# Kernel tuning notes

Hardware: AMD Instinct MI355X
Metric: run time of the kernel (lower is better)

## Reference

```python
import jax, jax.numpy as jnp
import numpy as np
import math

NUM_HEADS = 16
SEGMENT_SIZE = 256
DILATION_RATE = 2


def _hilbert_curve(n):
    if n == 1:
        return [(0, 0)]
    m = n // 2
    sub = _hilbert_curve(m)
    pts = [(y, x) for (x, y) in sub]
    pts += [(x, y + m) for (x, y) in sub]
    pts += [(x + m, y + m) for (x, y) in sub]
    pts += [(m - 1 - y + m, m - 1 - x) for (x, y) in sub]
    return pts


def generate_hilbert_curve_mapping(seq_len):
    grid = 2 ** int(math.ceil(math.log2(math.sqrt(seq_len))))
    pts = _hilbert_curve(grid)
    lin2hil = np.zeros(seq_len, dtype=np.int32)
    for h_idx, (x, y) in enumerate(pts[:seq_len]):
        lin = y * grid + x
        if lin < seq_len:
            lin2hil[lin] = h_idx
    return lin2hil


def setup_inputs() -> dict:
    key = jax.random.key(0)
    k1, k2, k3 = jax.random.split(key, 3)
    B, S, H = 1, 4096, 2048
    scale = H ** -0.5
    x = jax.random.normal(k1, (B, S, H), dtype=jnp.float32)
    w_qkv = jax.random.normal(k2, (3 * H, H), dtype=jnp.float32) * scale
    w_out = jax.random.normal(k3, (H, H), dtype=jnp.float32) * scale
    hilbert_map = jnp.asarray(generate_hilbert_curve_mapping(S))
    return {"x": x, "w_qkv": w_qkv, "w_out": w_out, "hilbert_map": hilbert_map}


def _kv_positions(S, seg, dil):
    # Union of per-segment dilated positions: seg_start + j*dil (< segment end).
    seg_starts = np.arange(0, S, seg)
    within = np.arange(0, seg, dil)
    return jnp.asarray((seg_starts[:, None] + within[None, :]).reshape(-1))


def reference(x, w_qkv, w_out, hilbert_map):
    B, S, H = x.shape
    nh = NUM_HEADS
    hd = H // nh
    qkv = x @ w_qkv.T                              # [B,S,3H]
    qkv = qkv.reshape(B, S, 3, nh, hd).transpose(2, 0, 3, 1, 4)  # [3,B,nh,S,hd]
    q, k, v = qkv[0], qkv[1], qkv[2]

    kv_pos = _kv_positions(S, SEGMENT_SIZE, DILATION_RATE)  # [Nk]
    gathered = hilbert_map[kv_pos]                 # Hilbert-mapped KV indices
    kg = k[:, :, gathered, :]                      # [B,nh,Nk,hd]
    vg = v[:, :, gathered, :]

    scale = 1.0 / jnp.sqrt(jnp.float32(hd))
    scores = jnp.einsum("bhmd,bhnd->bhmn", q, kg) * scale
    p = jax.nn.softmax(scores, axis=-1)
    acc = jnp.einsum("bhmn,bhnd->bhmd", p, vg)     # [B,nh,S,hd]

    # Scatter: out[:, :, hilbert_map[m], :] = acc[:, :, m, :]
    out = jnp.zeros_like(acc).at[:, :, hilbert_map, :].set(acc)
    out = out.transpose(0, 2, 1, 3).reshape(B, S, H)
    return out @ w_out.T
```

## Files before the change

kernel.cpp:

```cpp
#include <hip/hip_runtime.h>
#include <math.h>

#define S_LEN 4096
#define HID   2048
#define NH    16
#define HD    128
#define NKV   2048
#define KT    64
#define QBLK  256
#define NT    (NKV / KT)
#define QSCALE 0.12754103668587426f

typedef __attribute__((ext_vector_type(8))) _Float16 half8;
typedef __attribute__((ext_vector_type(4))) _Float16 half4;
typedef __attribute__((ext_vector_type(2))) __fp16 fp16x2;
typedef __attribute__((ext_vector_type(4))) float f32x4;
typedef __attribute__((ext_vector_type(16))) float f32x16;

#define GLB_AS __attribute__((address_space(1)))
#define LDS_AS __attribute__((address_space(3)))

#if __has_builtin(__builtin_amdgcn_exp2f)
#define EXP2(x) __builtin_amdgcn_exp2f(x)
#else
#define EXP2(x) exp2f(x)
#endif

__device__ __forceinline__ void gload16(const void* g, void* l) {
  __builtin_amdgcn_global_load_lds((GLB_AS const void*)g, (LDS_AS void*)l, 16, 0, 0);
}

__device__ __forceinline__ unsigned pkrtz(float a, float b) {
  union { fp16x2 h; unsigned u; } cv;
  cv.h = __builtin_amdgcn_cvt_pkrtz(a, b);
  return cv.u;
}

__global__ void k_build_idx(const int* __restrict__ hmap, int* __restrict__ gidx) {
  int i = blockIdx.x * 256 + threadIdx.x;
  if (i < NKV) gidx[i] = hmap[2 * i];
}

#define NX8  (S_LEN * HID / 8)
#define NW8  (3 * HID * HID / 8)
#define NO8  (HID * HID / 8)
__global__ void k_cvt_all(const float* __restrict__ x, const float* __restrict__ wq,
                          const float* __restrict__ wo, _Float16* __restrict__ x16,
                          _Float16* __restrict__ wq16, _Float16* __restrict__ wo16) {
  int i = blockIdx.x * 256 + threadIdx.x;
  const float* src; _Float16* dst; int j;
  if (i < NX8)            { src = x;  dst = x16;  j = i; }
  else if (i < NX8 + NW8) { src = wq; dst = wq16; j = i - NX8; }
  else                    { src = wo; dst = wo16; j = i - NX8 - NW8; }
  float4 a = ((const float4*)src)[2 * j];
  float4 b = ((const float4*)src)[2 * j + 1];
  half8 h;
  h[0] = (_Float16)a.x; h[1] = (_Float16)a.y; h[2] = (_Float16)a.z; h[3] = (_Float16)a.w;
  h[4] = (_Float16)b.x; h[5] = (_Float16)b.y; h[6] = (_Float16)b.z; h[7] = (_Float16)b.w;
  ((half8*)dst)[j] = h;
}

__global__ __launch_bounds__(512, 2)
void k_gemm_qkv8(const _Float16* __restrict__ A, const _Float16* __restrict__ wqkv,
                 _Float16* __restrict__ q16, const int* __restrict__ gidx,
                 char* __restrict__ kimg, char* __restrict__ vtimg)
{
  extern __shared__ __align__(16) char lds[];
  const int tid = threadIdx.x;
  const int w = tid >> 6, lane = tid & 63;
  const int l15 = lane & 15, l4 = lane >> 4;
  const int wr = w >> 2, wc = w & 3;
  const int K = HID;

  const int bid = (blockIdx.x & 7) * 32 + (blockIdx.x >> 3);
  const bool qpart = bid < 128;
  int m0, n0;
  const _Float16* B;
  if (qpart) { int b = bid;       m0 = (b >> 3) * 256; n0 = (b & 7) * 256;  B = wqkv; }
  else       { int b = bid - 128; m0 = (b >> 4) * 256; n0 = (b & 15) * 256; B = wqkv + (size_t)HID * HID; }

  const int r8 = lane >> 3;
  const int sl = (lane & 7) ^ r8;
  const _Float16* ApA[2][2];
  const _Float16* BpB[2][2];
#pragma unroll
  for (int mh = 0; mh < 2; ++mh)
#pragma unroll
    for (int L = 0; L < 2; ++L) {
      int rel = L * 128 + mh * 64 + w * 8 + r8;
      int grow = qpart ? (m0 + rel) : gidx[m0 + rel];
      ApA[mh][L] = A + (size_t)grow * K + sl * 8;
    }
#pragma unroll
  for (int nh = 0; nh < 2; ++nh)
#pragma unroll
    for (int L = 0; L < 2; ++L) {
      int row = n0 + (L * 2 + (w >> 2)) * 64 + nh * 32 + (w & 3) * 8 + r8;
      BpB[nh][L] = B + (size_t)row * K + sl * 8;
    }

  const int sw0 = (l4 ^ (l15 & 7)) * 16;
  const int sw1 = ((4 + l4) ^ (l15 & 7)) * 16;
  const int rofs = l15 * 128;

  f32x4 acc[8][4];
#pragma unroll
  for (int i = 0; i < 8; ++i)
#pragma unroll
    for (int j = 0; j < 4; ++j) acc[i][j] = (f32x4){0.f, 0.f, 0.f, 0.f};
  half8 af[4][2], bf[2][2];

#define STG_A(MH, BUF, T)                                                       \
  do {                                                                          \
    gload16(ApA[MH][0] + (T) * 64, lds + (BUF)*65536 + (MH)*16384 + w * 1024);  \
    gload16(ApA[MH][1] + (T) * 64, lds + (BUF)*65536 + (MH)*16384 + 8192 + w * 1024); \
  } while (0)
#define STG_B(NH, BUF, T)                                                       \
  do {                                                                          \
    gload16(BpB[NH][0] + (T) * 64, lds + (BUF)*65536 + 32768 + (NH)*16384 + w * 1024); \
    gload16(BpB[NH][1] + (T) * 64, lds + (BUF)*65536 + 32768 + (NH)*16384 + 8192 + w * 1024); \
  } while (0)

#define PH(BUF, MH, NH, LA, LB, STG, WAITS)                                     \
  do {                                                                          \
    if (LA) {                                                                   \
      _Pragma("unroll")                                                         \
      for (int j = 0; j < 4; ++j) {                                             \
        af[j][0] = *(const half8*)(lds + (BUF)*65536 + (MH)*16384 + wr * 8192 + j * 2048 + rofs + sw0); \
        af[j][1] = *(const half8*)(lds + (BUF)*65536 + (MH)*16384 + wr * 8192 + j * 2048 + rofs + sw1); \
      }                                                                         \
    }                                                                           \
    if (LB) {                                                                   \
      _Pragma("unroll")                                                         \
      for (int jn = 0; jn < 2; ++jn) {                                          \
        bf[jn][0] = *(const half8*)(lds + (BUF)*65536 + 32768 + (NH)*16384 + wc * 4096 + jn * 2048 + rofs + sw0); \
        bf[jn][1] = *(const half8*)(lds + (BUF)*65536 + 32768 + (NH)*16384 + wc * 4096 + jn * 2048 + rofs + sw1); \
      }                                                                         \
    }                                                                           \
    STG;                                                                        \
    __builtin_amdgcn_s_barrier();                                               \
    __builtin_amdgcn_s_setprio(1);                                              \
    _Pragma("unroll")                                                           \
    for (int j = 0; j < 4; ++j)                                                 \
      _Pragma("unroll")                                                         \
      for (int jn = 0; jn < 2; ++jn)                                            \
        _Pragma("unroll")                                                       \
        for (int ks = 0; ks < 2; ++ks)                                          \
          acc[(MH)*4 + j][(NH)*2 + jn] = __builtin_amdgcn_mfma_f32_16x16x32_f16( \
              af[j][ks], bf[jn][ks], acc[(MH)*4 + j][(NH)*2 + jn], 0, 0, 0);    \
    __builtin_amdgcn_s_setprio(0);                                              \
    WAITS;                                                                      \
    __builtin_amdgcn_s_barrier();                                               \
  } while (0)

  STG_A(0, 0, 0); STG_B(1, 0, 0); STG_A(1, 0, 0); STG_B(0, 0, 0);
  STG_A(0, 1, 1); STG_B(1, 1, 1);
  asm volatile("s_waitcnt vmcnt(4)");
  __builtin_amdgcn_s_barrier();

  for (int i = 0; i < 15; ++i) {
    const int T1 = 2 * i + 1, T2 = 2 * i + 2, T3 = 2 * i + 3;
    PH(0, 0, 0, 1, 1, STG_A(1, 1, T1), (void)0);
    PH(0, 0, 1, 0, 1, STG_B(0, 1, T1), (void)0);
    PH(0, 1, 1, 1, 0, STG_A(0, 0, T2), (void)0);
    PH(0, 1, 0, 0, 1, STG_B(1, 0, T2), asm volatile("s_waitcnt vmcnt(4)"));
    PH(1, 0, 0, 1, 1, STG_A(1, 0, T2), (void)0);
    PH(1, 0, 1, 0, 1, STG_B(0, 0, T2), (void)0);
    PH(1, 1, 1, 1, 0, STG_A(0, 1, T3), (void)0);
    PH(1, 1, 0, 0, 1, STG_B(1, 1, T3), asm volatile("s_waitcnt vmcnt(4)"));
  }
  PH(0, 0, 0, 1, 1, STG_A(1, 1, 31), (void)0);
  PH(0, 0, 1, 0, 1, STG_B(0, 1, 31), (void)0);
  PH(0, 1, 1, 1, 0, (void)0, (void)0);
  PH(0, 1, 0, 0, 1, (void)0, asm volatile("s_waitcnt vmcnt(0)"));
  PH(1, 0, 0, 1, 1, (void)0, (void)0);
  PH(1, 0, 1, 0, 1, (void)0, (void)0);
  PH(1, 1, 1, 1, 0, (void)0, (void)0);
  PH(1, 1, 0, 0, 1, (void)0, (void)0);
#undef PH
#undef STG_A
#undef STG_B

#pragma unroll
  for (int mf = 0; mf < 8; ++mf)
#pragma unroll
    for (int nf = 0; nf < 4; ++nf)
#pragma unroll
      for (int e = 0; e < 4; ++e) {
        int row = m0 + wr * 128 + mf * 16 + l4 * 4 + e;
        int col = n0 + wc * 64 + nf * 16 + l15;
        _Float16 val = (_Float16)acc[mf][nf][e];
        if (qpart) {
          q16[(size_t)row * HID + col] = val;
        } else {
          int r = row - m0 + m0;
          int t = r >> 6, j = r & 63;
          if (col < HID) {
            int h = col >> 7, d = col & 127;
            int off = (h * 32 + t) * 16384 + ((j * 256 + 2 * d) ^ ((j & 7) << 4));
            *(_Float16*)(kimg + off) = val;
          } else {
            int nn = col - HID;
            int h = nn >> 7, d = nn & 127;
            int off = (h * 32 + t) * 16384 + ((d * 128 + 2 * j) ^ ((d & 7) << 4));
            *(_Float16*)(vtimg + off) = val;
          }
        }
      }
}

__global__ __launch_bounds__(256)
void k_gemm_out(const _Float16* __restrict__ A, const _Float16* __restrict__ B,
                float* __restrict__ C, int M, int N, int K)
{
  __shared__ __align__(16) char Asl[16384];
  __shared__ __align__(16) char Bsl[16384];
  const int tid = threadIdx.x;
  const int w = tid >> 6, lane = tid & 63;
  const int l15 = lane & 15, l4 = lane >> 4;
  const int m0 = blockIdx.y * 128, n0 = blockIdx.x * 128;
  const int wr = w >> 1, wc = w & 1;

  const int srow  = lane >> 3;
  const int kso   = ((lane & 7) ^ srow) * 8;
  const _Float16* Ap[4];
  const _Float16* Bp[4];
#pragma unroll
  for (int q = 0; q < 4; ++q) {
    int row = m0 + 32 * w + 8 * q + srow;
    Ap[q] = A + (size_t)row * K + kso;
    Bp[q] = B + (size_t)(n0 + 32 * w + 8 * q + srow) * K + kso;
  }

  f32x4 acc[4][4];
#pragma unroll
  for (int i = 0; i < 4; ++i)
#pragma unroll
    for (int j = 0; j < 4; ++j) acc[i][j] = (f32x4){0.f, 0.f, 0.f, 0.f};

#define STAGE_T(k0)                                                  \
  do {                                                               \
    _Pragma("unroll")                                                \
    for (int q = 0; q < 4; ++q) {                                    \
      gload16(Ap[q] + (k0), Asl + (4 * w + q) * 1024 + lane * 16);   \
      gload16(Bp[q] + (k0), Bsl + (4 * w + q) * 1024 + lane * 16);   \
    }                                                                \
  } while (0)

  STAGE_T(0);
  __syncthreads();

  const int nt = K >> 6;
  for (int t = 0; t < nt; ++t) {
    half8 af[4][2], bf[4][2];
#pragma unroll
    for (int mi = 0; mi < 4; ++mi) {
      int row = wr * 64 + mi * 16 + l15;
#pragma unroll
      for (int ks = 0; ks < 2; ++ks)
        af[mi][ks] = *(const half8*)(Asl + row * 128 + (((ks * 4 + l4) ^ (row & 7)) * 16));
    }
#pragma unroll
    for (int ni = 0; ni < 4; ++ni) {
      int row = wc * 64 + ni * 16 + l15;
#pragma unroll
      for (int ks = 0; ks < 2; ++ks)
        bf[ni][ks] = *(const half8*)(Bsl + row * 128 + (((ks * 4 + l4) ^ (row & 7)) * 16));
    }
    __syncthreads();
    if (t + 1 < nt) STAGE_T((t + 1) * 64);
    __builtin_amdgcn_s_setprio(1);
#pragma unroll
    for (int mi = 0; mi < 4; ++mi)
#pragma unroll
      for (int ni = 0; ni < 4; ++ni)
#pragma unroll
        for (int ks = 0; ks < 2; ++ks)
          acc[mi][ni] = __builtin_amdgcn_mfma_f32_16x16x32_f16(af[mi][ks], bf[ni][ks], acc[mi][ni], 0, 0, 0);
    __builtin_amdgcn_s_setprio(0);
    __syncthreads();
  }
#undef STAGE_T

  const int rbase = m0 + wr * 64 + l4 * 4;
  const int cbase = n0 + wc * 64 + l15;
#pragma unroll
  for (int mi = 0; mi < 4; ++mi)
#pragma unroll
    for (int ni = 0; ni < 4; ++ni)
#pragma unroll
      for (int e = 0; e < 4; ++e)
        C[(size_t)(rbase + mi * 16 + e) * N + cbase + ni * 16] = acc[mi][ni][e];
}

__global__ __launch_bounds__(512, 2)
void k_attn9(const _Float16* __restrict__ qmat, const char* __restrict__ kimg,
             const char* __restrict__ vtimg, const int* __restrict__ hmap,
             _Float16* __restrict__ att)
{
  extern __shared__ __align__(16) char lds[];
  const int tid = threadIdx.x;
  const int w = tid >> 6, lane = tid & 63;
  const int l31 = lane & 31;
  const bool hi = (lane >> 5) != 0;
  const int hib = hi ? 1 : 0;
  const int work = (blockIdx.x & 7) * 32 + (blockIdx.x >> 3);
  const int h  = work >> 4;
  const int q0 = (work & 15) * QBLK;

  half8 qf[8];
  {
    const int qrow = q0 + w * 32 + l31;
    const _Float16* qb = qmat + (size_t)qrow * HID + h * HD + hib * 8;
    const _Float16 qs = (_Float16)QSCALE;
#pragma unroll
    for (int dk = 0; dk < 8; ++dk) {
      half8 v = *(const half8*)(qb + 16 * dk);
#pragma unroll
      for (int q = 0; q < 8; ++q) v[q] *= qs;
      qf[dk] = v;
    }
  }

  const int swz = (l31 & 7) << 4;
  int koff[4], voff[4];
#pragma unroll
  for (int i = 0; i < 4; ++i) {
    koff[i] = l31 * 256 + ((i * 32 + hib * 16) ^ swz);
    voff[i] = 16384 + l31 * 128 + ((i * 32 + hib * 16) ^ swz);
  }

  const char* kbase = kimg  + (size_t)h * NT * 16384;
  const char* vbase = vtimg + (size_t)h * NT * 16384;

  f32x16 acc[4];
#pragma unroll
  for (int dt = 0; dt < 4; ++dt)
#pragma unroll
    for (int r = 0; r < 16; ++r) acc[dt][r] = 0.f;
  float lsum = 0.f;

#define STAGE(buf, t)                                                          \
  do {                                                                         \
    const char* ks_ = kbase + (size_t)(t) * 16384;                             \
    const char* vs_ = vbase + (size_t)(t) * 16384;                             \
    char* d_ = lds + (buf) * 32768;                                            \
    gload16(ks_ + w * 1024 + lane * 16,          d_ + w * 1024);               \
    gload16(ks_ + (8 + w) * 1024 + lane * 16,    d_ + (8 + w) * 1024);         \
    gload16(vs_ + w * 1024 + lane * 16,          d_ + 16384 + w * 1024);       \
    gload16(vs_ + (8 + w) * 1024 + lane * 16,    d_ + 16384 + (8 + w) * 1024); \
  } while (0)

#define SM_HALF(S, PPK)                                                        \
  do {                                                                         \
    float p_[16];                                                              \
    _Pragma("unroll")                                                          \
    for (int r = 0; r < 16; ++r) { p_[r] = EXP2((S)[r]); lsum += p_[r]; }      \
    _Pragma("unroll")                                                          \
    for (int rq = 0; rq < 4; ++rq)                                             \
      _Pragma("unroll")                                                        \
      for (int h2 = 0; h2 < 2; ++h2)                                           \
        PPK[rq][h2] = pkrtz(p_[4 * rq + 2 * h2], p_[4 * rq + 2 * h2 + 1]);     \
  } while (0)

#define PV_HALF(PPK, KSB, CUR)                                                 \
  do {                                                                         \
    _Pragma("unroll")                                                          \
    for (int k1 = 0; k1 < 2; ++k1) {                                           \
      unsigned send0 = hi ? PPK[2 * k1][0]     : PPK[2 * k1 + 1][0];           \
      unsigned send1 = hi ? PPK[2 * k1][1]     : PPK[2 * k1 + 1][1];           \
      unsigned recv0 = (unsigned)__shfl_xor((int)send0, 32);                   \
      unsigned recv1 = (unsigned)__shfl_xor((int)send1, 32);                   \
      unsigned self0 = hi ? PPK[2 * k1 + 1][0] : PPK[2 * k1][0];               \
      unsigned self1 = hi ? PPK[2 * k1 + 1][1] : PPK[2 * k1][1];               \
      union { unsigned u[4]; half8 hv; } pf;                                   \
      pf.u[0] = hi ? recv0 : self0;                                            \
      pf.u[1] = hi ? recv1 : self1;                                            \
      pf.u[2] = hi ? self0 : recv0;                                            \
      pf.u[3] = hi ? self1 : recv1;                                            \
      __builtin_amdgcn_s_setprio(1);                                           \
      _Pragma("unroll")                                                        \
      for (int dt = 0; dt < 4; ++dt) {                                         \
        half8 vf = *(const half8*)(lds + voff[(KSB) + k1] +                    \
                    ((CUR) * 32768 + dt * 4096));                              \
        acc[dt] = __builtin_amdgcn_mfma_f32_32x32x16_f16(vf, pf.hv, acc[dt], 0, 0, 0); \
      }                                                                        \
      __builtin_amdgcn_s_setprio(0);                                           \
    }                                                                          \
  } while (0)

#define QK_HALF(S, JT, CUR)                                                    \
  do {                                                                         \
    _Pragma("unroll")                                                          \
    for (int r = 0; r < 16; ++r) (S)[r] = 0.f;                                 \
    __builtin_amdgcn_s_setprio(1);                                             \
    _Pragma("unroll")                                                          \
    for (int dk = 0; dk < 8; ++dk) {                                           \
      half8 kf = *(const half8*)(lds + koff[dk & 3] +                          \
                  ((CUR) * 32768 + (JT) * 8192 + (dk >> 2) * 128));            \
      (S) = __builtin_amdgcn_mfma_f32_32x32x16_f16(kf, qf[dk], (S), 0, 0, 0);  \
    }                                                                          \
    __builtin_amdgcn_s_setprio(0);                                             \
  } while (0)

#define TILE(CUR, T)                                                           \
  do {                                                                         \
    if ((T) + 1 < NT) STAGE((CUR) ^ 1, (T) + 1);                               \
    f32x16 sA, sB;                                                             \
    QK_HALF(sA, 0, CUR);                                                       \
    QK_HALF(sB, 1, CUR);                                                       \
    unsigned PA[4][2], PB[4][2];                                               \
    SM_HALF(sA, PA);                                                           \
    PV_HALF(PA, 0, CUR);                                                       \
    SM_HALF(sB, PB);                                                           \
    PV_HALF(PB, 2, CUR);                                                       \
    asm volatile("s_waitcnt vmcnt(0)");                                        \
    __syncthreads();                                                           \
  } while (0)

  STAGE(0, 0);
  asm volatile("s_waitcnt vmcnt(0)");
  __syncthreads();

  for (int t = 0; t < NT; t += 2) {
    TILE(0, t);
    TILE(1, t + 1);
  }
#undef TILE
#undef QK_HALF
#undef PV_HALF
#undef SM_HALF
#undef STAGE

  float lt = lsum + __shfl_xor(lsum, 32);
  const float rl = 1.0f / lt;
  const int qrow = q0 + w * 32 + l31;
  const int srow = hmap[qrow];
  _Float16* ob = att + (size_t)srow * HID + h * HD;
#pragma unroll
  for (int dt = 0; dt < 4; ++dt)
#pragma unroll
    for (int rq = 0; rq < 4; ++rq) {
      const int d0 = dt * 32 + 8 * rq + 4 * hib;
      half4 o;
      o[0] = (_Float16)(acc[dt][4 * rq + 0] * rl);
      o[1] = (_Float16)(acc[dt][4 * rq + 1] * rl);
      o[2] = (_Float16)(acc[dt][4 * rq + 2] * rl);
      o[3] = (_Float16)(acc[dt][4 * rq + 3] * rl);
      *(half4*)(ob + d0) = o;
    }
}

extern "C" void kernel_launch(void* const* d_in, const int* in_sizes, int n_in,
                              void* d_out, int out_size, void* d_ws, size_t ws_size,
                              hipStream_t stream)
{
  const float* x     = (const float*)d_in[0];
  const float* w_qkv = (const float*)d_in[1];
  const float* w_out = (const float*)d_in[2];
  const int*   hmap  = (const int*)d_in[3];
  float* out = (float*)d_out;

  char* ws = (char*)d_ws;
  int* gidx = (int*)ws;                                          ws += 8192;
  _Float16* x16    = (_Float16*)ws;
  _Float16* att16  = (_Float16*)ws;                              ws += (size_t)S_LEN * HID * 2;
  _Float16* wqkv16 = (_Float16*)ws;                              ws += (size_t)3 * HID * HID * 2;
  _Float16* wout16 = (_Float16*)ws;                              ws += (size_t)HID * HID * 2;
  _Float16* q16    = (_Float16*)ws;                              ws += (size_t)S_LEN * HID * 2;
  char* kimg  = ws;                                              ws += (size_t)NH * NT * 16384;
  char* vtimg = ws;

  k_build_idx<<<8, 256, 0, stream>>>(hmap, gidx);
  k_cvt_all<<<(NX8 + NW8 + NO8 + 255) / 256, 256, 0, stream>>>(x, w_qkv, w_out,
                                                               x16, wqkv16, wout16);

  k_gemm_qkv8<<<256, 512, 131072, stream>>>(x16, wqkv16, q16, gidx, kimg, vtimg);

  k_attn9<<<NH * (S_LEN / QBLK), 512, 65536, stream>>>(q16, kimg, vtimg, hmap, att16);

  dim3 go(HID / 128, S_LEN / 128);
  k_gemm_out<<<go, 256, 0, stream>>>(att16, wout16, out, S_LEN, HID, HID);
}
```

Measured before the change: 213.5 us.

## Stagger attention warp groups and deepen K/V staging to four LDS buffers

The attention kernel now splits its eight waves into two groups. Even waves run whole tiles, while odd waves run out of phase: they finish the previous tile's second half and start the next tile's first half. The goal is to interleave softmax/exp work with MFMA across waves, ping-pong style. K/V staging moves from double to quadruple buffering with partial vmcnt waits and raw s_barrier, which doubles dynamic LDS to 128KB. That likely limits the kernel to one block per CU despite launch_bounds(512,2).

```diff
diff --git a/kernel.cpp b/kernel.cpp
--- a/kernel.cpp
+++ b/kernel.cpp
@@ -193,7 +193,7 @@
         if (qpart) {
           q16[(size_t)row * HID + col] = val;
         } else {
-          int r = row - m0 + m0;
+          int r = row;
           int t = r >> 6, j = r & 63;
           if (col < HID) {
             int h = col >> 7, d = col & 127;
@@ -294,9 +294,9 @@
 }
 
 __global__ __launch_bounds__(512, 2)
-void k_attn9(const _Float16* __restrict__ qmat, const char* __restrict__ kimg,
-             const char* __restrict__ vtimg, const int* __restrict__ hmap,
-             _Float16* __restrict__ att)
+void k_attn11(const _Float16* __restrict__ qmat, const char* __restrict__ kimg,
+              const char* __restrict__ vtimg, const int* __restrict__ hmap,
+              _Float16* __restrict__ att)
 {
   extern __shared__ __align__(16) char lds[];
   const int tid = threadIdx.x;
@@ -304,6 +304,7 @@
   const int l31 = lane & 31;
   const bool hi = (lane >> 5) != 0;
   const int hib = hi ? 1 : 0;
+  const int wodd = (__builtin_amdgcn_readfirstlane(tid >> 6) >> 2) & 1;
   const int work = (blockIdx.x & 7) * 32 + (blockIdx.x >> 3);
   const int h  = work >> 4;
   const int q0 = (work & 15) * QBLK;
@@ -339,6 +340,7 @@
 #pragma unroll
     for (int r = 0; r < 16; ++r) acc[dt][r] = 0.f;
   float lsum = 0.f;
+  f32x16 sB;
 
 #define STAGE(buf, t)                                                          \
   do {                                                                         \
@@ -403,30 +405,56 @@
     __builtin_amdgcn_s_setprio(0);                                             \
   } while (0)
 
-#define TILE(CUR, T)                                                           \
-  do {                                                                         \
-    if ((T) + 1 < NT) STAGE((CUR) ^ 1, (T) + 1);                               \
-    f32x16 sA, sB;                                                             \
-    QK_HALF(sA, 0, CUR);                                                       \
-    QK_HALF(sB, 1, CUR);                                                       \
+#define BODY_E(CUR)                                                            \
+  do {                                                                         \
+    f32x16 sA2, sB2;                                                           \
     unsigned PA[4][2], PB[4][2];                                               \
-    SM_HALF(sA, PA);                                                           \
-    PV_HALF(PA, 0, CUR);                                                       \
-    SM_HALF(sB, PB);                                                           \
-    PV_HALF(PB, 2, CUR);                                                       \
-    asm volatile("s_waitcnt vmcnt(0)");                                        \
-    __syncthreads();                                                           \
+    QK_HALF(sA2, 0, CUR); QK_HALF(sB2, 1, CUR);                                \
+    SM_HALF(sA2, PA); PV_HALF(PA, 0, CUR);                                     \
+    SM_HALF(sB2, PB); PV_HALF(PB, 2, CUR);                                     \
+  } while (0)
+
+#define ODD_TAIL(CP)                                                           \
+  do {                                                                         \
+    unsigned PB[4][2];                                                         \
+    SM_HALF(sB, PB); PV_HALF(PB, 2, CP);                                       \
+  } while (0)
+
+#define ODD_HEAD(CN)                                                           \
+  do {                                                                         \
+    f32x16 sA;                                                                 \
+    unsigned PA[4][2];                                                         \
+    QK_HALF(sA, 0, CN); SM_HALF(sA, PA); PV_HALF(PA, 0, CN);                   \
+    QK_HALF(sB, 1, CN);                                                        \
+  } while (0)
+
+#define STEP(CE, CP, CN, STG, WAITS, DOE, DOPREV, DOCUR)                       \
+  do {                                                                         \
+    STG;                                                                       \
+    WAITS;                                                                     \
+    __builtin_amdgcn_s_barrier();                                              \
+    if (!wodd) { if (DOE) BODY_E(CE); }                                        \
+    else { if (DOPREV) ODD_TAIL(CP); if (DOCUR) ODD_HEAD(CN); }                \
+    __builtin_amdgcn_s_barrier();                                              \
   } while (0)
 
   STAGE(0, 0);
-  asm volatile("s_waitcnt vmcnt(0)");
-  __syncthreads();
-
-  for (int t = 0; t < NT; t += 2) {
-    TILE(0, t);
-    TILE(1, t + 1);
+  STAGE(1, 1);
+  STEP(0, 0, 0, STAGE(2, 2), asm volatile("s_waitcnt vmcnt(8)" ::: "memory"), 1, 0, 1);
+  STEP(1, 0, 1, STAGE(3, 3), asm volatile("s_waitcnt vmcnt(8)" ::: "memory"), 1, 1, 1);
+  for (int s = 2; s <= 26; s += 4) {
+    STEP(2, 1, 2, STAGE(0, s + 2), asm volatile("s_waitcnt vmcnt(8)" ::: "memory"), 1, 1, 1);
+    STEP(3, 2, 3, STAGE(1, s + 3), asm volatile("s_waitcnt vmcnt(8)" ::: "memory"), 1, 1, 1);
+    STEP(0, 3, 0, STAGE(2, s + 4), asm volatile("s_waitcnt vmcnt(8)" ::: "memory"), 1, 1, 1);
+    STEP(1, 0, 1, STAGE(3, s + 5), asm volatile("s_waitcnt vmcnt(8)" ::: "memory"), 1, 1, 1);
   }
-#undef TILE
+  STEP(2, 1, 2, (void)0, asm volatile("s_waitcnt vmcnt(4)" ::: "memory"), 1, 1, 1);
+  STEP(3, 2, 3, (void)0, asm volatile("s_waitcnt vmcnt(0)" ::: "memory"), 1, 1, 1);
+  STEP(0, 3, 0, (void)0, (void)0, 0, 1, 0);
+#undef STEP
+#undef BODY_E
+#undef ODD_TAIL
+#undef ODD_HEAD
 #undef QK_HALF
 #undef PV_HALF
 #undef SM_HALF
@@ -477,7 +505,7 @@
 
   k_gemm_qkv8<<<256, 512, 131072, stream>>>(x16, wqkv16, q16, gidx, kimg, vtimg);
 
-  k_attn9<<<NH * (S_LEN / QBLK), 512, 65536, stream>>>(q16, kimg, vtimg, hmap, att16);
+  k_attn11<<<NH * (S_LEN / QBLK), 512, 131072, stream>>>(q16, kimg, vtimg, hmap, att16);
 
   dim3 go(HID / 128, S_LEN / 128);
   k_gemm_out<<<go, 256, 0, stream>>>(att16, wout16, out, S_LEN, HID, HID);
```

Result: slower. 224.8 us (+5.3%).
